# Optimization experiments

Measured on AMD Instinct MI355X. Metric: run time of the kernel, lower is better.

The kernel has to match this reference:

```python
import jax, jax.numpy as jnp
import numpy as np


def setup_inputs() -> dict:
    key = jax.random.key(0)
    ks = jax.random.split(key, 6)
    B, C, D, H, O = 4096, 64, 512, 1024, 1
    z = jax.random.normal(ks[0], (B, D), dtype=jnp.float32)
    company_id = jax.random.randint(ks[1], (B,), 0, C)
    # PyTorch Linear default init ~ U(-1/sqrt(fan_in), 1/sqrt(fan_in)); use scaled normals for simplicity
    W1 = jax.random.normal(ks[2], (C, D, H), dtype=jnp.float32) / np.sqrt(D)
    b1 = jax.random.normal(ks[3], (C, H), dtype=jnp.float32) * 0.01
    W2 = jax.random.normal(ks[4], (C, H, O), dtype=jnp.float32) / np.sqrt(H)
    b2 = jax.random.normal(ks[5], (C, O), dtype=jnp.float32) * 0.01
    return {"z": z, "company_id": company_id, "W1": W1, "b1": b1, "W2": W2, "b2": b2}


def reference(z, company_id, W1, b1, W2, b2):
    # Faithful to original: every company head is applied to the full batch,
    # then the single needed row per sample is gathered (dropout is identity in eval).
    # h: [B, C, H]
    h = jnp.einsum("bd,cdh->bch", z, W1) + b1[None, :, :]
    h = jax.nn.gelu(h, approximate=False)  # nn.GELU default = exact erf GELU
    # all_outputs: [B, C, O]
    all_outputs = jnp.einsum("bch,cho->bco", h, W2) + b2[None, :, :]
    # gather the per-sample company row -> [B, O]
    outputs = jnp.take_along_axis(all_outputs, company_id[:, None, None], axis=1)[:, 0, :]
    return outputs
```

## Files before the change

kernel.cpp:

```cpp
#include <hip/hip_runtime.h>

typedef float f32x4 __attribute__((ext_vector_type(4)));
typedef short s16x8 __attribute__((ext_vector_type(8)));

#define B_SZ 4096
#define C_N  64
#define D_K  512
#define H_N  1024
#define HS   4
#define MAXR 112
#define MF   7
#define KSTEPS 16
#define DEPTH 8
#define LDS_BYTES (MAXR*D_K*2 + 512)

__device__ __forceinline__ short f2bf(float f){
  unsigned u = __float_as_uint(f);
  u += 0x7FFFu + ((u >> 16) & 1u);
  return (short)(u >> 16);
}
__device__ __forceinline__ float erf_fast(float x){
  float ax = fabsf(x);
  float t = __builtin_amdgcn_rcpf(1.0f + 0.3275911f * ax);
  float p = t * (0.254829592f + t * (-0.284496736f + t * (1.421413741f +
            t * (-1.453152027f + t * 1.061405429f))));
  float r = 1.0f - p * __expf(-ax * ax);
  return copysignf(r, x);
}
__device__ __forceinline__ float gelu_exact(float x){
  return 0.5f * x * (1.0f + erf_fast(x * 0.70710678118654752f));
}

__global__ void k_prep(const int* __restrict__ cid, const float* __restrict__ b2,
                       int* __restrict__ offsets, int* __restrict__ bucket,
                       float* __restrict__ out){
  __shared__ int hist[C_N];
  const int tid = threadIdx.x;
  if (tid < C_N) hist[tid] = 0;
  __syncthreads();
  for (int i = tid; i < B_SZ; i += 1024) atomicAdd(&hist[cid[i]], 1);
  __syncthreads();
  if (tid < 64){
    int v = hist[tid];
    int x = v;
    #pragma unroll
    for (int d = 1; d < 64; d <<= 1){
      int y = __shfl_up(x, d, 64);
      if (tid >= d) x += y;
    }
    offsets[tid] = x - v;
    if (tid == 63) offsets[64] = x;
    hist[tid] = x - v;
  }
  __syncthreads();
  for (int i = tid; i < B_SZ; i += 1024){
    int c = cid[i];
    int p = atomicAdd(&hist[c], 1);
    bucket[p] = i;
    out[i] = b2[c];
  }
}

__global__ __launch_bounds__(1024, 4) void k_main(
    const float* __restrict__ z, const float* __restrict__ W1,
    const float* __restrict__ b1, const float* __restrict__ W2,
    const int* __restrict__ offsets, const int* __restrict__ bucket,
    float* __restrict__ out)
{
  extern __shared__ char smem[];
  s16x8* A_lds   = (s16x8*)smem;
  float* partial = (float*)(smem + MAXR * D_K * 2);

  const int flat = blockIdx.x;
  const int c  = flat & 63;
  const int hs = flat >> 6;
  const int off_c = offsets[c];
  const int n_c   = offsets[c + 1] - off_c;
  if (n_c == 0) return;

  const int tid  = threadIdx.x;
  const int lane = tid & 63, wave = tid >> 6;
  const int l15 = lane & 15, l4 = lane >> 4;
  const int h0 = hs * 256 + wave * 16;
  const float* Wc = W1 + (size_t)c * D_K * H_N;
  const float* bp_base = Wc + (size_t)(l4 * 8) * H_N + h0 + l15;

  const int hcol = c * H_N + h0 + l15;
  const float b1v = b1[hcol];
  const float w2v = W2[hcol];

  for (int rb = 0; rb < n_c; rb += MAXR){
    const int rows = (n_c - rb < MAXR) ? (n_c - rb) : MAXR;
    const int M = (rows + 15) >> 4;

    __syncthreads();

    float fb[DEPTH][8];
    #pragma unroll
    for (int s = 0; s < DEPTH; ++s){
      #pragma unroll
      for (int e = 0; e < 8; ++e)
        fb[s][e] = bp_base[(size_t)(s * 32 + e) * H_N];
    }

    if (tid < 128) partial[tid] = 0.0f;

    for (int i = 0; i < M; ++i){
      int unit = tid + 1024 * i;
      int rg = rb + i * 16 + l15;
      int k  = wave * 32 + l4 * 8;
      float4 a = make_float4(0.f,0.f,0.f,0.f), b = make_float4(0.f,0.f,0.f,0.f);
      if (rg < n_c){
        const float* zp = z + (size_t)bucket[off_c + rg] * D_K + k;
        a = *(const float4*)zp;
        b = *(const float4*)(zp + 4);
      }
      s16x8 v;
      v[0]=f2bf(a.x); v[1]=f2bf(a.y); v[2]=f2bf(a.z); v[3]=f2bf(a.w);
      v[4]=f2bf(b.x); v[5]=f2bf(b.y); v[6]=f2bf(b.z); v[7]=f2bf(b.w);
      A_lds[unit] = v;
    }
    __syncthreads();

    f32x4 acc[MF];
    #pragma unroll
    for (int m = 0; m < MF; ++m) acc[m] = 0;

    #pragma unroll
    for (int t = 0; t < KSTEPS; ++t){
      const int sl = t & (DEPTH - 1);
      s16x8 bf;
      #pragma unroll
      for (int e = 0; e < 8; ++e) bf[e] = f2bf(fb[sl][e]);
      #pragma unroll
      for (int m = 0; m < MF; ++m){
        if (m >= M) break;
        s16x8 af = A_lds[(m * 16 + t) * 64 + lane];
        acc[m] = __builtin_amdgcn_mfma_f32_16x16x32_bf16(af, bf, acc[m], 0, 0, 0);
      }
      if (t < KSTEPS - DEPTH){
        #pragma unroll
        for (int e = 0; e < 8; ++e)
          fb[sl][e] = bp_base[(size_t)((t + DEPTH) * 32 + e) * H_N];
      }
    }

    #pragma unroll
    for (int m = 0; m < MF; ++m){
      if (m >= M) break;
      #pragma unroll
      for (int r = 0; r < 4; ++r){
        float s = gelu_exact(acc[m][r] + b1v) * w2v;
        s += __shfl_xor(s, 1, 64);
        s += __shfl_xor(s, 2, 64);
        s += __shfl_xor(s, 4, 64);
        s += __shfl_xor(s, 8, 64);
        int row = m * 16 + l4 * 4 + r;
        if (l15 == 0 && row < rows){
          atomicAdd(&partial[row], s);
        }
      }
    }
    __syncthreads();
    for (int r = tid; r < rows; r += 1024){
      atomicAdd(&out[bucket[off_c + rb + r]], partial[r]);
    }
  }
}

extern "C" void kernel_launch(void* const* d_in, const int* in_sizes, int n_in,
                              void* d_out, int out_size, void* d_ws, size_t ws_size,
                              hipStream_t stream){
  const float* z  = (const float*)d_in[0];
  const int*   cid= (const int*)  d_in[1];
  const float* W1 = (const float*)d_in[2];
  const float* b1 = (const float*)d_in[3];
  const float* W2 = (const float*)d_in[4];
  const float* b2 = (const float*)d_in[5];
  float* out = (float*)d_out;

  int* ws      = (int*)d_ws;
  int* offsets = ws;
  int* bucket  = ws + 128;

  (void)hipFuncSetAttribute((const void*)k_main,
                            hipFuncAttributeMaxDynamicSharedMemorySize, LDS_BYTES);

  k_prep<<<1, 1024, 0, stream>>>(cid, b2, offsets, bucket, out);
  k_main<<<C_N * HS, 1024, LDS_BYTES, stream>>>(z, W1, b1, W2, offsets, bucket, out);
}
```

Measured before the change: 52.31 us.

## Pre-pack gathered z to bf16 and switch to 32x32 MFMA register-fed kernel

```diff
diff --git a/kernel.cpp b/kernel.cpp
--- a/kernel.cpp
+++ b/kernel.cpp
@@ -1,18 +1,15 @@
 #include <hip/hip_runtime.h>
 
-typedef float f32x4 __attribute__((ext_vector_type(4)));
-typedef short s16x8 __attribute__((ext_vector_type(8)));
+typedef float f32x16 __attribute__((ext_vector_type(16)));
+typedef short s16x8  __attribute__((ext_vector_type(8)));
 
 #define B_SZ 4096
 #define C_N  64
 #define D_K  512
 #define H_N  1024
-#define HS   4
-#define MAXR 112
-#define MF   7
-#define KSTEPS 16
-#define DEPTH 8
-#define LDS_BYTES (MAXR*D_K*2 + 512)
+#define MF   4
+#define TSTEPS 32
+#define ZP_OFF_BYTES 32768
 
 __device__ __forceinline__ short f2bf(float f){
   unsigned u = __float_as_uint(f);
@@ -61,110 +58,111 @@
   }
 }
 
-__global__ __launch_bounds__(1024, 4) void k_main(
-    const float* __restrict__ z, const float* __restrict__ W1,
+__global__ void k_zpack(const float* __restrict__ z, const int* __restrict__ bucket,
+                        short* __restrict__ zp){
+  int u = blockIdx.x * 256 + threadIdx.x;
+  int slot = u >> 6;
+  int k0 = (u & 63) * 8;
+  const float* src = z + (size_t)bucket[slot] * D_K + k0;
+  float4 a = *(const float4*)src;
+  float4 b = *(const float4*)(src + 4);
+  s16x8 v;
+  v[0]=f2bf(a.x); v[1]=f2bf(a.y); v[2]=f2bf(a.z); v[3]=f2bf(a.w);
+  v[4]=f2bf(b.x); v[5]=f2bf(b.y); v[6]=f2bf(b.z); v[7]=f2bf(b.w);
+  *(s16x8*)(zp + ((size_t)slot << 9) + k0) = v;
+}
+
+__global__ __launch_bounds__(256, 2) void k_main(
+    const short* __restrict__ zp, const float* __restrict__ W1,
     const float* __restrict__ b1, const float* __restrict__ W2,
     const int* __restrict__ offsets, const int* __restrict__ bucket,
     float* __restrict__ out)
 {
-  extern __shared__ char smem[];
-  s16x8* A_lds   = (s16x8*)smem;
-  float* partial = (float*)(smem + MAXR * D_K * 2);
-
+  __shared__ float partial[128];
   const int flat = blockIdx.x;
-  const int c  = flat & 63;
-  const int hs = flat >> 6;
+  const int c = flat & 63, slice = flat >> 6;
   const int off_c = offsets[c];
-  const int n_c   = offsets[c + 1] - off_c;
+  const int n_c = offsets[c + 1] - off_c;
   if (n_c == 0) return;
 
   const int tid  = threadIdx.x;
   const int lane = tid & 63, wave = tid >> 6;
-  const int l15 = lane & 15, l4 = lane >> 4;
-  const int h0 = hs * 256 + wave * 16;
-  const float* Wc = W1 + (size_t)c * D_K * H_N;
-  const float* bp_base = Wc + (size_t)(l4 * 8) * H_N + h0 + l15;
+  const int l31 = lane & 31, lhi = lane >> 5;
+  const int hcol = slice * 128 + wave * 32 + l31;
+  const float* Wc = W1 + (size_t)c * D_K * H_N + hcol;
+  const float b1v = b1[c * H_N + hcol];
+  const float w2v = W2[c * H_N + hcol];
 
-  const int hcol = c * H_N + h0 + l15;
-  const float b1v = b1[hcol];
-  const float w2v = W2[hcol];
-
-  for (int rb = 0; rb < n_c; rb += MAXR){
-    const int rows = (n_c - rb < MAXR) ? (n_c - rb) : MAXR;
-    const int M = (rows + 15) >> 4;
-
+  for (int rb = 0; rb < n_c; rb += 128){
+    if (tid < 128) partial[tid] = 0.0f;
     __syncthreads();
 
-    float fb[DEPTH][8];
+    float fb[4][8];
     #pragma unroll
-    for (int s = 0; s < DEPTH; ++s){
+    for (int s = 0; s < 4; ++s){
       #pragma unroll
       for (int e = 0; e < 8; ++e)
-        fb[s][e] = bp_base[(size_t)(s * 32 + e) * H_N];
+        fb[s][e] = Wc[(size_t)(s * 16 + lhi * 8 + e) * H_N];
     }
 
-    if (tid < 128) partial[tid] = 0.0f;
+    s16x8 af[2][MF];
+    #pragma unroll
+    for (int m = 0; m < MF; ++m){
+      int row = rb + m * 32 + l31;
+      af[0][m] = (row < n_c)
+        ? *(const s16x8*)(zp + ((size_t)(off_c + row) << 9) + lhi * 8)
+        : (s16x8)0;
+    }
 
-    for (int i = 0; i < M; ++i){
-      int unit = tid + 1024 * i;
-      int rg = rb + i * 16 + l15;
-      int k  = wave * 32 + l4 * 8;
-      float4 a = make_float4(0.f,0.f,0.f,0.f), b = make_float4(0.f,0.f,0.f,0.f);
-      if (rg < n_c){
-        const float* zp = z + (size_t)bucket[off_c + rg] * D_K + k;
-        a = *(const float4*)zp;
-        b = *(const float4*)(zp + 4);
-      }
-      s16x8 v;
-      v[0]=f2bf(a.x); v[1]=f2bf(a.y); v[2]=f2bf(a.z); v[3]=f2bf(a.w);
-      v[4]=f2bf(b.x); v[5]=f2bf(b.y); v[6]=f2bf(b.z); v[7]=f2bf(b.w);
-      A_lds[unit] = v;
-    }
-    __syncthreads();
-
-    f32x4 acc[MF];
+    f32x16 acc[MF];
     #pragma unroll
     for (int m = 0; m < MF; ++m) acc[m] = 0;
 
-    #pragma unroll
-    for (int t = 0; t < KSTEPS; ++t){
-      const int sl = t & (DEPTH - 1);
+    #pragma unroll 4
+    for (int t = 0; t < TSTEPS; ++t){
+      const int sl = t & 3, cur = t & 1;
       s16x8 bf;
       #pragma unroll
       for (int e = 0; e < 8; ++e) bf[e] = f2bf(fb[sl][e]);
-      #pragma unroll
-      for (int m = 0; m < MF; ++m){
-        if (m >= M) break;
-        s16x8 af = A_lds[(m * 16 + t) * 64 + lane];
-        acc[m] = __builtin_amdgcn_mfma_f32_16x16x32_bf16(af, bf, acc[m], 0, 0, 0);
+      if (t < TSTEPS - 1){
+        #pragma unroll
+        for (int m = 0; m < MF; ++m){
+          int row = rb + m * 32 + l31;
+          af[cur ^ 1][m] = (row < n_c)
+            ? *(const s16x8*)(zp + ((size_t)(off_c + row) << 9) + (t + 1) * 16 + lhi * 8)
+            : (s16x8)0;
+        }
       }
-      if (t < KSTEPS - DEPTH){
+      if (t < TSTEPS - 4){
         #pragma unroll
         for (int e = 0; e < 8; ++e)
-          fb[sl][e] = bp_base[(size_t)((t + DEPTH) * 32 + e) * H_N];
+          fb[sl][e] = Wc[(size_t)((t + 4) * 16 + lhi * 8 + e) * H_N];
       }
+      #pragma unroll
+      for (int m = 0; m < MF; ++m)
+        acc[m] = __builtin_amdgcn_mfma_f32_32x32x16_bf16(af[cur][m], bf, acc[m], 0, 0, 0);
     }
 
     #pragma unroll
     for (int m = 0; m < MF; ++m){
-      if (m >= M) break;
       #pragma unroll
-      for (int r = 0; r < 4; ++r){
+      for (int r = 0; r < 16; ++r){
+        int row = rb + m * 32 + (r & 3) + 8 * (r >> 2) + 4 * lhi;
         float s = gelu_exact(acc[m][r] + b1v) * w2v;
         s += __shfl_xor(s, 1, 64);
         s += __shfl_xor(s, 2, 64);
         s += __shfl_xor(s, 4, 64);
         s += __shfl_xor(s, 8, 64);
-        int row = m * 16 + l4 * 4 + r;
-        if (l15 == 0 && row < rows){
-          atomicAdd(&partial[row], s);
-        }
+        s += __shfl_xor(s, 16, 64);
+        if (l31 == 0 && row < n_c)
+          atomicAdd(&partial[row - rb], s);
       }
     }
     __syncthreads();
-    for (int r = tid; r < rows; r += 1024){
+    int rows = n_c - rb; if (rows > 128) rows = 128;
+    for (int r = tid; r < rows; r += 256)
       atomicAdd(&out[bucket[off_c + rb + r]], partial[r]);
-    }
+    __syncthreads();
   }
 }
 
@@ -179,13 +177,12 @@
   const float* b2 = (const float*)d_in[5];
   float* out = (float*)d_out;
 
-  int* ws      = (int*)d_ws;
-  int* offsets = ws;
-  int* bucket  = ws + 128;
+  int*   ws      = (int*)d_ws;
+  int*   offsets = ws;
+  int*   bucket  = ws + 128;
+  short* zp      = (short*)((char*)d_ws + ZP_OFF_BYTES);
 
-  (void)hipFuncSetAttribute((const void*)k_main,
-                            hipFuncAttributeMaxDynamicSharedMemorySize, LDS_BYTES);
-
-  k_prep<<<1, 1024, 0, stream>>>(cid, b2, offsets, bucket, out);
-  k_main<<<C_N * HS, 1024, LDS_BYTES, stream>>>(z, W1, b1, W2, offsets, bucket, out);
+  k_prep <<<1, 1024, 0, stream>>>(cid, b2, offsets, bucket, out);
+  k_zpack<<<1024, 256, 0, stream>>>(z, bucket, zp);
+  k_main <<<C_N * 8, 256, 0, stream>>>(zp, W1, b1, W2, offsets, bucket, out);
 }
```

Result: slower. 56.59 us (+8.2%).
